# Performance work log

Hardware: AMD Instinct MI355X
Metric: run time of the kernel (lower is better)

Reference implementation:

```python
import jax, jax.numpy as jnp
import numpy as np

NH = 8      # num_heads
NP_ = 4     # num_points

def setup_inputs() -> dict:
    key = jax.random.key(0)
    ks = jax.random.split(key, 12)
    B, N, C = 8, 4096, 256
    query = jax.random.normal(ks[0], (B, N, C), jnp.float32)
    value = jax.random.normal(ks[1], (B, N, C), jnp.float32)
    reference_points = jax.random.uniform(ks[2], (B, N, 2), jnp.float32)
    xav = lambda k, i, o: jax.random.normal(k, (i, o), jnp.float32) * np.sqrt(2.0 / (i + o)).astype(np.float32)
    W_off = jax.random.normal(ks[3], (C, NH * NP_ * 2), jnp.float32) * 0.02  # small offsets (orig inits to 0)
    b_off = jax.random.normal(ks[4], (NH * NP_ * 2,), jnp.float32) * 0.02
    W_attn = xav(ks[5], C, NH * NP_)
    b_attn = jnp.zeros((NH * NP_,), jnp.float32)
    W_val = xav(ks[6], C, C)
    b_val = jnp.zeros((C,), jnp.float32)
    W_out = xav(ks[7], C, C)
    b_out = jnp.zeros((C,), jnp.float32)
    return dict(query=query, value=value, reference_points=reference_points,
                W_off=W_off, b_off=b_off, W_attn=W_attn, b_attn=b_attn,
                W_val=W_val, b_val=b_val, W_out=W_out, b_out=b_out)

def _deform_attn(query, value, reference_points, W_off, b_off, W_attn, b_attn, W_val, b_val, W_out, b_out):
    B, N, C = query.shape
    HW = value.shape[1]
    H = W = int(np.sqrt(HW))  # static
    hd = C // NH
    # value projection -> [B, NH, H*W, hd]
    vals = (value @ W_val + b_val).reshape(B, H, W, NH, hd)
    vals = vals.transpose(0, 3, 1, 2, 4).reshape(B, NH, H * W, hd)
    # offsets [B,N,NH,P,2] in [-0.5,0.5]; attention weights softmax over P
    off = jnp.tanh((query @ W_off + b_off).reshape(B, N, NH, NP_, 2)) * 0.5
    attn = jax.nn.softmax((query @ W_attn + b_attn).reshape(B, N, NH, NP_), axis=-1)
    # sampling locations in [0,1], then grid coords in [-1,1] (x=width, y=height)
    loc = jnp.clip(reference_points[:, :, None, None, :] + off, 0.0, 1.0)
    g = loc * 2.0 - 1.0
    # torch grid_sample, align_corners=False: pixel = (g+1)*size/2 - 0.5
    x = (g[..., 0] + 1.0) * (W * 0.5) - 0.5
    y = (g[..., 1] + 1.0) * (H * 0.5) - 0.5
    x0f = jnp.floor(x); y0f = jnp.floor(y)
    wx1 = x - x0f; wx0 = 1.0 - wx1
    wy1 = y - y0f; wy0 = 1.0 - wy1
    x0 = x0f.astype(jnp.int32); x1 = x0 + 1
    y0 = y0f.astype(jnp.int32); y1 = y0 + 1

    def corner(xi, yi, w):  # xi,yi,w: [B,N,NH,P]; zero padding outside
        valid = (xi >= 0) & (xi < W) & (yi >= 0) & (yi < H)
        idx = jnp.clip(yi, 0, H - 1) * W + jnp.clip(xi, 0, W - 1)
        idx_h = idx.transpose(0, 2, 1, 3).reshape(B, NH, N * NP_)      # [B,NH,N*P]
        gat = jnp.take_along_axis(vals, idx_h[..., None], axis=2)      # [B,NH,N*P,hd]
        wv = jnp.where(valid, w, 0.0).transpose(0, 2, 1, 3).reshape(B, NH, N * NP_)
        return gat * wv[..., None]

    sampled = (corner(x0, y0, wx0 * wy0) + corner(x1, y0, wx1 * wy0)
               + corner(x0, y1, wx0 * wy1) + corner(x1, y1, wx1 * wy1))
    sampled = sampled.reshape(B, NH, N, NP_, hd)
    attn_h = attn.transpose(0, 2, 1, 3)                                 # [B,NH,N,P]
    out = jnp.einsum('bhnpd,bhnp->bnhd', sampled, attn_h).reshape(B, N, C)
    return out @ W_out + b_out  # dropout is identity in eval

def reference(query, value, reference_points, W_off, b_off, W_attn, b_attn, W_val, b_val, W_out, b_out):
    return _deform_attn(query, value, reference_points, W_off, b_off, W_attn, b_attn, W_val, b_val, W_out, b_out)
```

## Files before the change

### kernel.cpp

```cpp
#include <hip/hip_runtime.h>
#include <math.h>

#define NHEAD 8
#define NPT 4
#define HDIM 32
#define IMG 64
#define CDIM 256
#define NQ 4096
#define BATCH 8
#define MTOT (BATCH * NQ)

typedef __attribute__((ext_vector_type(8))) short bf16x8;
typedef __attribute__((ext_vector_type(4))) float f32x4;

__device__ __forceinline__ unsigned short f2b(float f) {
    union { float f; unsigned u; } v; v.f = f;
    unsigned r = (v.u + 0x7FFFu + ((v.u >> 16) & 1u)) >> 16;
    return (unsigned short)r;
}
__device__ __forceinline__ float b2f(unsigned short u) {
    union { unsigned u; float f; } v; v.u = ((unsigned)u) << 16;
    return v.f;
}

#define SWZ(row, col)   ((col) ^ (((row) & 7) << 3))

__device__ __forceinline__ void gload16(const void* src, void* ldsbase) {
    __builtin_amdgcn_global_load_lds(
        (const __attribute__((address_space(1))) void*)src,
        (__attribute__((address_space(3))) void*)ldsbase, 16, 0, 0);
}


__global__ __launch_bounds__(256)
void cvt_value_kernel(const float* __restrict__ in, unsigned short* __restrict__ out)
{
    const int n8 = MTOT * 256 / 8;
    for (int i = blockIdx.x * 256 + threadIdx.x; i < n8; i += 2048 * 256) {
        const float4 a = ((const float4*)in)[i * 2];
        const float4 b = ((const float4*)in)[i * 2 + 1];
        unsigned short us[8] = { f2b(a.x), f2b(a.y), f2b(a.z), f2b(a.w),
                                 f2b(b.x), f2b(b.y), f2b(b.z), f2b(b.w) };
        ((uint4*)out)[i] = *(const uint4*)us;
    }
}

__global__ __launch_bounds__(256)
void cvt_weights_kernel(const float* __restrict__ Wv, const float* __restrict__ Wo,
                        const float* __restrict__ Woff, const float* __restrict__ Wattn,
                        const float* __restrict__ boff, const float* __restrict__ battn,
                        unsigned short* __restrict__ Wv_t, unsigned short* __restrict__ Wo_t,
                        unsigned short* __restrict__ Wl_h, unsigned short* __restrict__ Wl_l,
                        float* __restrict__ bias_lin)
{
    int tid = blockIdx.x * 256 + threadIdx.x;
    int n = tid & 255, k = tid >> 8;
    Wv_t[n * 256 + k] = f2b(Wv[k * 256 + n]);
    Wo_t[n * 256 + k] = f2b(Wo[k * 256 + n]);
    if (tid < 128 * 256) {
        int nn = tid >> 8;
        int kk = tid & 255;
        float v = (nn < 64) ? Woff[kk * 64 + nn]
                : (nn < 96) ? Wattn[kk * 32 + (nn - 64)] : 0.f;
        unsigned short hi = f2b(v);
        unsigned short lo = f2b(v - b2f(hi));
        Wl_h[nn * 256 + kk] = hi;
        Wl_l[nn * 256 + kk] = lo;
    }
    if (tid < 128)
        bias_lin[tid] = (tid < 64) ? boff[tid] : (tid < 96) ? battn[tid - 64] : 0.f;
}

__global__ __launch_bounds__(256)
void fused_gemms_kernel(const unsigned short* __restrict__ value_bf,
                        const float* __restrict__ query,
                        const unsigned short* __restrict__ Wv_t,
                        const unsigned short* __restrict__ Wl_h,
                        const unsigned short* __restrict__ Wl_l,
                        const float* __restrict__ b_val,
                        const float* __restrict__ bias_lin,
                        unsigned short* __restrict__ projv,
                        float* __restrict__ lin)
{
    __shared__ char smem[32768];

    const int tid  = threadIdx.x;
    const int lane = tid & 63;
    const int wid  = tid >> 6;
    const int wr = (wid >> 1) * 64;
    const int wc = (wid & 1) * 64;
    const int l15 = lane & 15;
    const int lk  = (lane >> 4) * 8;

    f32x4 acc[4][4];
    #pragma unroll
    for (int m = 0; m < 4; ++m)
        #pragma unroll
        for (int n = 0; n < 4; ++n)
            #pragma unroll
            for (int r = 0; r < 4; ++r) acc[m][n][r] = 0.f;

    if (blockIdx.x >= 256) {
        unsigned short (*As)[64] = (unsigned short(*)[64])smem;
        unsigned short (*Bs)[64] = (unsigned short(*)[64])(smem + 16384);
        const int bx = blockIdx.x - 256;
        const int gm = ((bx & 7) << 12) + (((bx >> 3) & 31) << 7);
        const int gn = (bx >> 8) << 7;
        const int rl  = lane >> 3;
        const int ch  = (lane & 7) ^ rl;

        for (int k0 = 0; k0 < 256; k0 += 64) {
            #pragma unroll
            for (int it = 0; it < 4; ++it) {
                const int br = it * 32 + wid * 8;
                gload16(&Wv_t[(size_t)(gn + br + rl) * 256 + k0 + ch * 8], &Bs[br][0]);
                gload16(&value_bf[(size_t)(gm + br + rl) * 256 + k0 + ch * 8], &As[br][0]);
            }
            __syncthreads();

            #pragma unroll
            for (int kk = 0; kk < 64; kk += 32) {
                bf16x8 a[4], b[4];
                #pragma unroll
                for (int m = 0; m < 4; ++m) {
                    const int r = wr + m * 16 + l15;
                    a[m] = *(const bf16x8*)&As[r][SWZ(r, kk + lk)];
                }
                #pragma unroll
                for (int n = 0; n < 4; ++n) {
                    const int r = wc + n * 16 + l15;
                    b[n] = *(const bf16x8*)&Bs[r][SWZ(r, kk + lk)];
                }
                #pragma unroll
                for (int m = 0; m < 4; ++m)
                    #pragma unroll
                    for (int n = 0; n < 4; ++n)
                        acc[m][n] = __builtin_amdgcn_mfma_f32_16x16x32_bf16(a[m], b[n], acc[m][n], 0, 0, 0);
            }
            __syncthreads();
        }

        const int cr = (lane >> 4) * 4;
        #pragma unroll
        for (int n = 0; n < 4; ++n) {
            const int col = gn + wc + n * 16 + l15;
            const float bv = b_val[col];
            #pragma unroll
            for (int m = 0; m < 4; ++m)
                #pragma unroll
                for (int r = 0; r < 4; ++r) {
                    const int row = gm + wr + m * 16 + cr + r;
                    projv[(size_t)row * 256 + col] = f2b(acc[m][n][r] + bv);
                }
        }
    } else {
        float (*Aq)[32] = (float(*)[32])smem;
        unsigned short (*Bh)[32] = (unsigned short(*)[32])(smem + 16384);
        unsigned short (*Bl)[32] = (unsigned short(*)[32])(smem + 24576);
        const int lbx = blockIdx.x;
        const int gm = ((lbx & 7) << 12) + ((lbx >> 3) << 7);
        const int rla = lane >> 3;
        const int ca  = (lane & 7) ^ rla;
        const int rsb = lane >> 2;
        const int cb  = (lane & 3) ^ (rsb & 3);

        for (int k0 = 0; k0 < 256; k0 += 32) {
            #pragma unroll
            for (int i = 0; i < 4; ++i) {
                const int ar = wid * 32 + i * 8;
                gload16(&query[(size_t)(gm + ar + rla) * 256 + k0 + ca * 4], &Aq[ar][0]);
            }
            #pragma unroll
            for (int i = 0; i < 2; ++i) {
                const int br = wid * 32 + i * 16;
                gload16(&Wl_h[(size_t)(br + rsb) * 256 + k0 + cb * 8], &Bh[br][0]);
                gload16(&Wl_l[(size_t)(br + rsb) * 256 + k0 + cb * 8], &Bl[br][0]);
            }
            __syncthreads();

            bf16x8 ah[4], al[4];
            #pragma unroll
            for (int m = 0; m < 4; ++m) {
                const int r = wr + m * 16 + l15;
                const int c0 = ((lk >> 2) ^ (r & 7)) << 2;
                const int c1 = (((lk >> 2) + 1) ^ (r & 7)) << 2;
                const f32x4 qa = *(const f32x4*)&Aq[r][c0];
                const f32x4 qb = *(const f32x4*)&Aq[r][c1];
                float f[8] = {qa.x, qa.y, qa.z, qa.w, qb.x, qb.y, qb.z, qb.w};
                unsigned short h[8], l[8];
                #pragma unroll
                for (int j = 0; j < 8; ++j) {
                    h[j] = f2b(f[j]);
                    l[j] = f2b(f[j] - b2f(h[j]));
                }
                ah[m] = *(const bf16x8*)h;
                al[m] = *(const bf16x8*)l;
            }

            const int nN = (wc == 0) ? 4 : 2;
            #pragma unroll
            for (int n = 0; n < 4; ++n) {
                if (n >= nN) break;
                const int r = wc + n * 16 + l15;
                const int c = ((lk >> 3) ^ (r & 3)) << 3;
                const bf16x8 bh = *(const bf16x8*)&Bh[r][c];
                const bf16x8 bl = *(const bf16x8*)&Bl[r][c];
                #pragma unroll
                for (int m = 0; m < 4; ++m) {
                    acc[m][n] = __builtin_amdgcn_mfma_f32_16x16x32_bf16(ah[m], bh, acc[m][n], 0, 0, 0);
                    acc[m][n] = __builtin_amdgcn_mfma_f32_16x16x32_bf16(ah[m], bl, acc[m][n], 0, 0, 0);
                    acc[m][n] = __builtin_amdgcn_mfma_f32_16x16x32_bf16(al[m], bh, acc[m][n], 0, 0, 0);
                }
            }
            __syncthreads();
        }

        const int cr = (lane >> 4) * 4;
        #pragma unroll
        for (int n = 0; n < 4; ++n) {
            const int col = wc + n * 16 + l15;
            if (col < 96) {
                const float bv = bias_lin[col];
                #pragma unroll
                for (int m = 0; m < 4; ++m)
                    #pragma unroll
                    for (int r = 0; r < 4; ++r) {
                        const int row = gm + wr + m * 16 + cr + r;
                        lin[(size_t)row * 96 + col] = acc[m][n][r] + bv;
                    }
            }
        }
    }
}

__global__ __launch_bounds__(256)
void gemm_out_kernel(const unsigned short* __restrict__ Ap,
                     const unsigned short* __restrict__ Bt,
                     const float* __restrict__ bias,
                     float* __restrict__ C)
{
    __shared__ unsigned short As[128][64];
    __shared__ unsigned short Bs[128][64];

    const int tid  = threadIdx.x;
    const int lane = tid & 63;
    const int wid  = tid >> 6;
    const int gm = ((blockIdx.x & 7) << 12) + ((blockIdx.x >> 3) << 7);
    const int gn = blockIdx.y * 128;
    const int wr = (wid >> 1) * 64;
    const int wc = (wid & 1) * 64;
    const int l15 = lane & 15;
    const int lk  = (lane >> 4) * 8;
    const int rl  = lane >> 3;
    const int ch  = (lane & 7) ^ rl;

    f32x4 acc[4][4];
    #pragma unroll
    for (int m = 0; m < 4; ++m)
        #pragma unroll
        for (int n = 0; n < 4; ++n)
            #pragma unroll
            for (int r = 0; r < 4; ++r) acc[m][n][r] = 0.f;

    for (int k0 = 0; k0 < 256; k0 += 64) {
        #pragma unroll
        for (int it = 0; it < 4; ++it) {
            const int br = it * 32 + wid * 8;
            gload16(&Bt[(size_t)(gn + br + rl) * 256 + k0 + ch * 8], &Bs[br][0]);
            gload16(&Ap[(size_t)(gm + br + rl) * 256 + k0 + ch * 8], &As[br][0]);
        }
        __syncthreads();

        #pragma unroll
        for (int kk = 0; kk < 64; kk += 32) {
            bf16x8 a[4], b[4];
            #pragma unroll
            for (int m = 0; m < 4; ++m) {
                const int r = wr + m * 16 + l15;
                a[m] = *(const bf16x8*)&As[r][SWZ(r, kk + lk)];
            }
            #pragma unroll
            for (int n = 0; n < 4; ++n) {
                const int r = wc + n * 16 + l15;
                b[n] = *(const bf16x8*)&Bs[r][SWZ(r, kk + lk)];
            }
            #pragma unroll
            for (int m = 0; m < 4; ++m)
                #pragma unroll
                for (int n = 0; n < 4; ++n)
                    acc[m][n] = __builtin_amdgcn_mfma_f32_16x16x32_bf16(a[m], b[n], acc[m][n], 0, 0, 0);
        }
        __syncthreads();
    }

    const int cr = (lane >> 4) * 4;
    #pragma unroll
    for (int n = 0; n < 4; ++n) {
        const int col = gn + wc + n * 16 + l15;
        const float bv = bias[col];
        #pragma unroll
        for (int m = 0; m < 4; ++m)
            #pragma unroll
            for (int r = 0; r < 4; ++r) {
                const int row = gm + wr + m * 16 + cr + r;
                C[(size_t)row * 256 + col] = acc[m][n][r] + bv;
            }
    }
}

__global__ __launch_bounds__(256)
void sample_gather_kernel(const unsigned short* __restrict__ projv,
                          const float* __restrict__ lin,
                          const float* __restrict__ refp,
                          unsigned short* __restrict__ sampled)
{
    __shared__ float4 s_w[8][32];
    __shared__ unsigned s_xy[8][32];

    const int i = blockIdx.x;
    const int b = i & 7;
    const int bn0 = (b << 12) + ((i >> 3) << 3);
    const int t = threadIdx.x;

    {
        const int sub = t >> 5;
        const int q = t & 31;
        const int h = q >> 2;
        const int p = q & 3;
        const int bn = bn0 + sub;
        const float2 rp = *(const float2*)&refp[(size_t)bn * 2];
        const float2 ol = *(const float2*)&lin[(size_t)bn * 96 + h * 8 + p * 2];
        const float al  = lin[(size_t)bn * 96 + 64 + q];

        float mx = al;
        mx = fmaxf(mx, __shfl_xor(mx, 1));
        mx = fmaxf(mx, __shfl_xor(mx, 2));
        float e = expf(al - mx);
        float s = e;
        s += __shfl_xor(s, 1);
        s += __shfl_xor(s, 2);
        const float aw = e / s;

        const float lx = fminf(fmaxf(rp.x + tanhf(ol.x) * 0.5f, 0.f), 1.f);
        const float ly = fminf(fmaxf(rp.y + tanhf(ol.y) * 0.5f, 0.f), 1.f);
        const float x = lx * (float)IMG - 0.5f;
        const float y = ly * (float)IMG - 0.5f;
        const float x0f = floorf(x), y0f = floorf(y);
        const int x0 = (int)x0f, y0 = (int)y0f;
        const float wx1 = x - x0f, wx0 = 1.f - wx1;
        const float wy1 = y - y0f, wy0 = 1.f - wy1;
        const bool vx0 = (x0 >= 0), vx1 = (x0 + 1 < IMG);
        const bool vy0 = (y0 >= 0), vy1 = (y0 + 1 < IMG);
        float4 w;
        w.x = (vx0 && vy0) ? wx0 * wy0 * aw : 0.f;
        w.y = (vx1 && vy0) ? wx1 * wy0 * aw : 0.f;
        w.z = (vx0 && vy1) ? wx0 * wy1 * aw : 0.f;
        w.w = (vx1 && vy1) ? wx1 * wy1 * aw : 0.f;
        const int x0c = min(max(x0, 0), IMG - 1), x1c = min(max(x0 + 1, 0), IMG - 1);
        const int y0c = min(max(y0, 0), IMG - 1), y1c = min(max(y0 + 1, 0), IMG - 1);
        s_w[sub][q] = w;
        s_xy[sub][q] = (unsigned)x0c | ((unsigned)x1c << 8) | ((unsigned)y0c << 16) | ((unsigned)y1c << 24);
    }
    __syncthreads();

    const int l = t & 63;
    const int h2 = l >> 3;
    const int cp = l & 7;
    const unsigned short* vbase = projv + ((size_t)b << 20) + h2 * HDIM + cp * 4;

    #pragma unroll
    for (int pass = 0; pass < 2; ++pass) {
        const int sub = (t >> 6) + pass * 4;
        const int bn = bn0 + sub;

        float a0 = 0.f, a1 = 0.f, a2 = 0.f, a3 = 0.f;
        #pragma unroll
        for (int p = 0; p < 4; ++p) {
            const float4 w = s_w[sub][h2 * 4 + p];
            const unsigned xy = s_xy[sub][h2 * 4 + p];
            const int x0 = xy & 255, x1 = (xy >> 8) & 255;
            const int y0 = (xy >> 16) & 255, y1 = xy >> 24;
            const uint2 u00 = *(const uint2*)&vbase[(((y0 << 6) + x0) << 8)];
            const uint2 u01 = *(const uint2*)&vbase[(((y0 << 6) + x1) << 8)];
            const uint2 u10 = *(const uint2*)&vbase[(((y1 << 6) + x0) << 8)];
            const uint2 u11 = *(const uint2*)&vbase[(((y1 << 6) + x1) << 8)];
            a0 += w.x * b2f((unsigned short)(u00.x & 0xffff)) + w.y * b2f((unsigned short)(u01.x & 0xffff))
                + w.z * b2f((unsigned short)(u10.x & 0xffff)) + w.w * b2f((unsigned short)(u11.x & 0xffff));
            a1 += w.x * b2f((unsigned short)(u00.x >> 16)) + w.y * b2f((unsigned short)(u01.x >> 16))
                + w.z * b2f((unsigned short)(u10.x >> 16)) + w.w * b2f((unsigned short)(u11.x >> 16));
            a2 += w.x * b2f((unsigned short)(u00.y & 0xffff)) + w.y * b2f((unsigned short)(u01.y & 0xffff))
                + w.z * b2f((unsigned short)(u10.y & 0xffff)) + w.w * b2f((unsigned short)(u11.y & 0xffff));
            a3 += w.x * b2f((unsigned short)(u00.y >> 16)) + w.y * b2f((unsigned short)(u01.y >> 16))
                + w.z * b2f((unsigned short)(u10.y >> 16)) + w.w * b2f((unsigned short)(u11.y >> 16));
        }
        uint2 outp;
        outp.x = (unsigned)f2b(a0) | ((unsigned)f2b(a1) << 16);
        outp.y = (unsigned)f2b(a2) | ((unsigned)f2b(a3) << 16);
        *(uint2*)&sampled[(size_t)bn * 256 + h2 * HDIM + cp * 4] = outp;
    }
}

extern "C" void kernel_launch(void* const* d_in, const int* in_sizes, int n_in,
                              void* d_out, int out_size, void* d_ws, size_t ws_size,
                              hipStream_t stream)
{
    const float* query  = (const float*)d_in[0];
    const float* value  = (const float*)d_in[1];
    const float* refp   = (const float*)d_in[2];
    const float* W_off  = (const float*)d_in[3];
    const float* b_off  = (const float*)d_in[4];
    const float* W_attn = (const float*)d_in[5];
    const float* b_attn = (const float*)d_in[6];
    const float* W_val  = (const float*)d_in[7];
    const float* b_val  = (const float*)d_in[8];
    const float* W_out  = (const float*)d_in[9];
    const float* b_out  = (const float*)d_in[10];
    float* out = (float*)d_out;

    char* ws = (char*)d_ws;
    unsigned short* projv    = (unsigned short*)ws; ws += (size_t)MTOT * 256 * 2;
    unsigned short* sampled  = (unsigned short*)ws; ws += (size_t)MTOT * 256 * 2;
    unsigned short* value_bf = (unsigned short*)ws; ws += (size_t)MTOT * 256 * 2;
    float*          lin      = (float*)ws;          ws += (size_t)MTOT * 96 * 4;
    unsigned short* Wv_t     = (unsigned short*)ws; ws += 256 * 256 * 2;
    unsigned short* Wo_t     = (unsigned short*)ws; ws += 256 * 256 * 2;
    unsigned short* Wl_h     = (unsigned short*)ws; ws += 128 * 256 * 2;
    unsigned short* Wl_l     = (unsigned short*)ws; ws += 128 * 256 * 2;
    float*          bias_lin = (float*)ws;          ws += 128 * 4;

    dim3 blk(256);

    cvt_weights_kernel<<<dim3(256), blk, 0, stream>>>(W_val, W_out, W_off, W_attn, b_off, b_attn,
                                                      Wv_t, Wo_t, Wl_h, Wl_l, bias_lin);
    cvt_value_kernel<<<dim3(2048), blk, 0, stream>>>(value, value_bf);

    fused_gemms_kernel<<<dim3(768), blk, 0, stream>>>(value_bf, query, Wv_t, Wl_h, Wl_l,
                                                      b_val, bias_lin, projv, lin);

    sample_gather_kernel<<<dim3(MTOT / 8), blk, 0, stream>>>(projv, lin, refp, sampled);

    gemm_out_kernel<<<dim3(MTOT / 128, 2), blk, 0, stream>>>(sampled, Wo_t, b_out, out);
}
```

Before: 72.07 us.

## Fuse value bf16 conversion into GEMM and split query GEMM along K

Removes the separate value fp32-to-bf16 conversion kernel: the value-projection GEMM now loads fp32 value directly, converts it in registers and writes swizzled bf16 into LDS. This drops a full write and re-read of a bf16 copy of value. The query linear GEMM is split into two K halves, giving 1024 blocks instead of 768 for better load balance. The two partial results and the bias are summed in the sampling kernel. The trade-off is synchronous global loads for the A operand instead of async LDS loads, plus extra traffic for the doubled lin buffer.

```diff
diff --git a/kernel.cpp b/kernel.cpp
--- a/kernel.cpp
+++ b/kernel.cpp
@@ -31,19 +31,6 @@
         (__attribute__((address_space(3))) void*)ldsbase, 16, 0, 0);
 }
 
-
-__global__ __launch_bounds__(256)
-void cvt_value_kernel(const float* __restrict__ in, unsigned short* __restrict__ out)
-{
-    const int n8 = MTOT * 256 / 8;
-    for (int i = blockIdx.x * 256 + threadIdx.x; i < n8; i += 2048 * 256) {
-        const float4 a = ((const float4*)in)[i * 2];
-        const float4 b = ((const float4*)in)[i * 2 + 1];
-        unsigned short us[8] = { f2b(a.x), f2b(a.y), f2b(a.z), f2b(a.w),
-                                 f2b(b.x), f2b(b.y), f2b(b.z), f2b(b.w) };
-        ((uint4*)out)[i] = *(const uint4*)us;
-    }
-}
 
 __global__ __launch_bounds__(256)
 void cvt_weights_kernel(const float* __restrict__ Wv, const float* __restrict__ Wo,
@@ -72,17 +59,16 @@
 }
 
 __global__ __launch_bounds__(256)
-void fused_gemms_kernel(const unsigned short* __restrict__ value_bf,
+void fused_gemms_kernel(const float* __restrict__ value,
                         const float* __restrict__ query,
                         const unsigned short* __restrict__ Wv_t,
                         const unsigned short* __restrict__ Wl_h,
                         const unsigned short* __restrict__ Wl_l,
                         const float* __restrict__ b_val,
-                        const float* __restrict__ bias_lin,
                         unsigned short* __restrict__ projv,
                         float* __restrict__ lin)
 {
-    __shared__ char smem[32768];
+    __shared__ __align__(16) char smem[32768];
 
     const int tid  = threadIdx.x;
     const int lane = tid & 63;
@@ -92,6 +78,9 @@
     const int l15 = lane & 15;
     const int lk  = (lane >> 4) * 8;
 
+    const int b = blockIdx.x & 7;
+    const int j = blockIdx.x >> 3;
+
     f32x4 acc[4][4];
     #pragma unroll
     for (int m = 0; m < 4; ++m)
@@ -100,12 +89,11 @@
             #pragma unroll
             for (int r = 0; r < 4; ++r) acc[m][n][r] = 0.f;
 
-    if (blockIdx.x >= 256) {
+    if (j < 64) {
         unsigned short (*As)[64] = (unsigned short(*)[64])smem;
         unsigned short (*Bs)[64] = (unsigned short(*)[64])(smem + 16384);
-        const int bx = blockIdx.x - 256;
-        const int gm = ((bx & 7) << 12) + (((bx >> 3) & 31) << 7);
-        const int gn = (bx >> 8) << 7;
+        const int gm = (b << 12) + ((j & 31) << 7);
+        const int gn = (j >> 5) << 7;
         const int rl  = lane >> 3;
         const int ch  = (lane & 7) ^ rl;
 
@@ -114,13 +102,25 @@
             for (int it = 0; it < 4; ++it) {
                 const int br = it * 32 + wid * 8;
                 gload16(&Wv_t[(size_t)(gn + br + rl) * 256 + k0 + ch * 8], &Bs[br][0]);
-                gload16(&value_bf[(size_t)(gm + br + rl) * 256 + k0 + ch * 8], &As[br][0]);
+            }
+            #pragma unroll
+            for (int it = 0; it < 4; ++it) {
+                const int chunk = it * 256 + tid;
+                const int row = chunk >> 3;
+                const int kc  = (chunk & 7) << 3;
+                const float4* src = (const float4*)&value[(size_t)(gm + row) * 256 + k0 + kc];
+                const float4 a = src[0], bb = src[1];
+                float f[8] = {a.x, a.y, a.z, a.w, bb.x, bb.y, bb.z, bb.w};
+                unsigned short h[8];
+                #pragma unroll
+                for (int jj = 0; jj < 8; ++jj) h[jj] = f2b(f[jj]);
+                *(uint4*)&As[row][SWZ(row, kc)] = *(const uint4*)h;
             }
             __syncthreads();
 
             #pragma unroll
             for (int kk = 0; kk < 64; kk += 32) {
-                bf16x8 a[4], b[4];
+                bf16x8 a[4], bv[4];
                 #pragma unroll
                 for (int m = 0; m < 4; ++m) {
                     const int r = wr + m * 16 + l15;
@@ -129,13 +129,13 @@
                 #pragma unroll
                 for (int n = 0; n < 4; ++n) {
                     const int r = wc + n * 16 + l15;
-                    b[n] = *(const bf16x8*)&Bs[r][SWZ(r, kk + lk)];
+                    bv[n] = *(const bf16x8*)&Bs[r][SWZ(r, kk + lk)];
                 }
                 #pragma unroll
                 for (int m = 0; m < 4; ++m)
                     #pragma unroll
                     for (int n = 0; n < 4; ++n)
-                        acc[m][n] = __builtin_amdgcn_mfma_f32_16x16x32_bf16(a[m], b[n], acc[m][n], 0, 0, 0);
+                        acc[m][n] = __builtin_amdgcn_mfma_f32_16x16x32_bf16(a[m], bv[n], acc[m][n], 0, 0, 0);
             }
             __syncthreads();
         }
@@ -144,27 +144,28 @@
         #pragma unroll
         for (int n = 0; n < 4; ++n) {
             const int col = gn + wc + n * 16 + l15;
-            const float bv = b_val[col];
+            const float bvv = b_val[col];
             #pragma unroll
             for (int m = 0; m < 4; ++m)
                 #pragma unroll
                 for (int r = 0; r < 4; ++r) {
                     const int row = gm + wr + m * 16 + cr + r;
-                    projv[(size_t)row * 256 + col] = f2b(acc[m][n][r] + bv);
+                    projv[(size_t)row * 256 + col] = f2b(acc[m][n][r] + bvv);
                 }
         }
     } else {
         float (*Aq)[32] = (float(*)[32])smem;
         unsigned short (*Bh)[32] = (unsigned short(*)[32])(smem + 16384);
         unsigned short (*Bl)[32] = (unsigned short(*)[32])(smem + 24576);
-        const int lbx = blockIdx.x;
-        const int gm = ((lbx & 7) << 12) + ((lbx >> 3) << 7);
+        const int u  = j - 64;
+        const int gm = (b << 12) + ((u & 31) << 7);
+        const int kq = u >> 5;
         const int rla = lane >> 3;
         const int ca  = (lane & 7) ^ rla;
         const int rsb = lane >> 2;
         const int cb  = (lane & 3) ^ (rsb & 3);
 
-        for (int k0 = 0; k0 < 256; k0 += 32) {
+        for (int k0 = kq * 128; k0 < kq * 128 + 128; k0 += 32) {
             #pragma unroll
             for (int i = 0; i < 4; ++i) {
                 const int ar = wid * 32 + i * 8;
@@ -189,9 +190,9 @@
                 float f[8] = {qa.x, qa.y, qa.z, qa.w, qb.x, qb.y, qb.z, qb.w};
                 unsigned short h[8], l[8];
                 #pragma unroll
-                for (int j = 0; j < 8; ++j) {
-                    h[j] = f2b(f[j]);
-                    l[j] = f2b(f[j] - b2f(h[j]));
+                for (int jj = 0; jj < 8; ++jj) {
+                    h[jj] = f2b(f[jj]);
+                    l[jj] = f2b(f[jj] - b2f(h[jj]));
                 }
                 ah[m] = *(const bf16x8*)h;
                 al[m] = *(const bf16x8*)l;
@@ -215,18 +216,18 @@
             __syncthreads();
         }
 
+        float* dst = lin + (size_t)kq * MTOT * 96;
         const int cr = (lane >> 4) * 4;
         #pragma unroll
         for (int n = 0; n < 4; ++n) {
             const int col = wc + n * 16 + l15;
             if (col < 96) {
-                const float bv = bias_lin[col];
                 #pragma unroll
                 for (int m = 0; m < 4; ++m)
                     #pragma unroll
                     for (int r = 0; r < 4; ++r) {
                         const int row = gm + wr + m * 16 + cr + r;
-                        lin[(size_t)row * 96 + col] = acc[m][n][r] + bv;
+                        dst[(size_t)row * 96 + col] = acc[m][n][r];
                     }
             }
         }
@@ -311,6 +312,7 @@
 __global__ __launch_bounds__(256)
 void sample_gather_kernel(const unsigned short* __restrict__ projv,
                           const float* __restrict__ lin,
+                          const float* __restrict__ bias_lin,
                           const float* __restrict__ refp,
                           unsigned short* __restrict__ sampled)
 {
@@ -329,8 +331,14 @@
         const int p = q & 3;
         const int bn = bn0 + sub;
         const float2 rp = *(const float2*)&refp[(size_t)bn * 2];
-        const float2 ol = *(const float2*)&lin[(size_t)bn * 96 + h * 8 + p * 2];
-        const float al  = lin[(size_t)bn * 96 + 64 + q];
+        const size_t base0 = (size_t)bn * 96;
+        const size_t base1 = (size_t)MTOT * 96 + base0;
+        const float2 o0 = *(const float2*)&lin[base0 + h * 8 + p * 2];
+        const float2 o1 = *(const float2*)&lin[base1 + h * 8 + p * 2];
+        const float2 ob = *(const float2*)&bias_lin[h * 8 + p * 2];
+        const float olx = o0.x + o1.x + ob.x;
+        const float oly = o0.y + o1.y + ob.y;
+        const float al  = lin[base0 + 64 + q] + lin[base1 + 64 + q] + bias_lin[64 + q];
 
         float mx = al;
         mx = fmaxf(mx, __shfl_xor(mx, 1));
@@ -341,8 +349,8 @@
         s += __shfl_xor(s, 2);
         const float aw = e / s;
 
-        const float lx = fminf(fmaxf(rp.x + tanhf(ol.x) * 0.5f, 0.f), 1.f);
-        const float ly = fminf(fmaxf(rp.y + tanhf(ol.y) * 0.5f, 0.f), 1.f);
+        const float lx = fminf(fmaxf(rp.x + tanhf(olx) * 0.5f, 0.f), 1.f);
+        const float ly = fminf(fmaxf(rp.y + tanhf(oly) * 0.5f, 0.f), 1.f);
         const float x = lx * (float)IMG - 0.5f;
         const float y = ly * (float)IMG - 0.5f;
         const float x0f = floorf(x), y0f = floorf(y);
@@ -420,8 +428,7 @@
     char* ws = (char*)d_ws;
     unsigned short* projv    = (unsigned short*)ws; ws += (size_t)MTOT * 256 * 2;
     unsigned short* sampled  = (unsigned short*)ws; ws += (size_t)MTOT * 256 * 2;
-    unsigned short* value_bf = (unsigned short*)ws; ws += (size_t)MTOT * 256 * 2;
-    float*          lin      = (float*)ws;          ws += (size_t)MTOT * 96 * 4;
+    float*          lin      = (float*)ws;          ws += (size_t)2 * MTOT * 96 * 4;
     unsigned short* Wv_t     = (unsigned short*)ws; ws += 256 * 256 * 2;
     unsigned short* Wo_t     = (unsigned short*)ws; ws += 256 * 256 * 2;
     unsigned short* Wl_h     = (unsigned short*)ws; ws += 128 * 256 * 2;
@@ -432,12 +439,11 @@
 
     cvt_weights_kernel<<<dim3(256), blk, 0, stream>>>(W_val, W_out, W_off, W_attn, b_off, b_attn,
                                                       Wv_t, Wo_t, Wl_h, Wl_l, bias_lin);
-    cvt_value_kernel<<<dim3(2048), blk, 0, stream>>>(value, value_bf);
-
-    fused_gemms_kernel<<<dim3(768), blk, 0, stream>>>(value_bf, query, Wv_t, Wl_h, Wl_l,
-                                                      b_val, bias_lin, projv, lin);
-
-    sample_gather_kernel<<<dim3(MTOT / 8), blk, 0, stream>>>(projv, lin, refp, sampled);
+
+    fused_gemms_kernel<<<dim3(1024), blk, 0, stream>>>(value, query, Wv_t, Wl_h, Wl_l,
+                                                       b_val, projv, lin);
+
+    sample_gather_kernel<<<dim3(MTOT / 8), blk, 0, stream>>>(projv, lin, bias_lin, refp, sampled);
 
     gemm_out_kernel<<<dim3(MTOT / 128, 2), blk, 0, stream>>>(sampled, Wo_t, b_out, out);
 }
```

New measurement: 70.15 us. 2.7% less time.
